# Kernel tuning notes

Measured on AMD Instinct MI355X. Metric: run time of the kernel, lower is better.

Reference implementation:

```python
import jax, jax.numpy as jnp
import numpy as np

B, T = 8, 16384
CLASSES, RC, EC = 256, 32, 256
NLAYERS = 40          # blocks(4) * layers(10)
DIL = 1024            # source uses 2**layers for every layer (faithful to code)
EPS = 1e-5


def _shift_right(x, d):
    # causal shift: y[t] = x[t-d], zero-padded
    return jnp.pad(x, ((0, 0), (0, 0), (d, 0)))[:, :, : x.shape[-1]]


def _conv1x1(x, w, b):
    # w: [out, in], x: [B, in, T]
    return jnp.einsum('oi,bit->bot', w, x) + b[None, :, None]


def _dconv2(x, w, b, d):
    # causal dilated conv, kernel 2: y[t] = w[:,:,0] x[t-d] + w[:,:,1] x[t] + b
    return (jnp.einsum('oi,bit->bot', w[:, :, 1], x)
            + jnp.einsum('oi,bit->bot', w[:, :, 0], _shift_right(x, d))
            + b[None, :, None])


def _bn(x, g, b):
    # training-mode BatchNorm1d: batch stats over (N, L)
    m = jnp.mean(x, axis=(0, 2), keepdims=True)
    v = jnp.var(x, axis=(0, 2), keepdims=True)
    return (x - m) * jax.lax.rsqrt(v + EPS) * g[None, :, None] + b[None, :, None]


def _mish(x):
    return x * jnp.tanh(jax.nn.softplus(x))


def setup_inputs() -> dict:
    key = jax.random.key(0)
    ks = jax.random.split(key, 16)
    n = jax.random.normal
    return {
        'x': n(ks[0], (B, CLASSES, T), jnp.float32),
        'start_w': n(ks[1], (RC, CLASSES), jnp.float32) * 0.05,
        'start_b': n(ks[2], (RC,), jnp.float32) * 0.05,
        'gt_w': n(ks[3], (NLAYERS, RC, RC, 2), jnp.float32) * 0.1,   # tanh branch
        'gt_b': n(ks[4], (NLAYERS, RC), jnp.float32) * 0.05,
        'gs_w': n(ks[5], (NLAYERS, RC, RC, 2), jnp.float32) * 0.1,   # sigmoid branch
        'gs_b': n(ks[6], (NLAYERS, RC), jnp.float32) * 0.05,
        'res_w': n(ks[7], (NLAYERS, RC, RC), jnp.float32) * 0.1,
        'res_b': n(ks[8], (NLAYERS, RC), jnp.float32) * 0.05,
        'bn_g': jnp.ones((NLAYERS, RC), jnp.float32),
        'bn_b': jnp.zeros((NLAYERS, RC), jnp.float32),
        'bn1_g': jnp.ones((RC,), jnp.float32),
        'bn1_b': jnp.zeros((RC,), jnp.float32),
        'e1_w': n(ks[9], (EC, RC), jnp.float32) * 0.1,
        'e1_b': n(ks[10], (EC,), jnp.float32) * 0.05,
        'bn2_g': jnp.ones((EC,), jnp.float32),
        'bn2_b': jnp.zeros((EC,), jnp.float32),
        'e2_w': n(ks[11], (CLASSES, EC), jnp.float32) * 0.05,
        'e2_b': n(ks[12], (CLASSES,), jnp.float32) * 0.05,
    }


def reference(x, start_w, start_b, gt_w, gt_b, gs_w, gs_b, res_w, res_b,
              bn_g, bn_b, bn1_g, bn1_b, e1_w, e1_b, bn2_g, bn2_b, e2_w, e2_b):
    # start_conv: CausalConv(classes, RC, k=1, shift=1) -> 1x1 conv on x shifted right by 1
    h = _conv1x1(_shift_right(x, 1), start_w, start_b)  # [B, RC, T]

    def step(carry, p):
        h, skip = carry
        gtw, gtb, gsw, gsb, rw, rb, bg, bb = p
        g = jnp.tanh(_dconv2(h, gtw, gtb, DIL)) * jax.nn.sigmoid(_dconv2(h, gsw, gsb, DIL))
        skip = skip + g
        h = h + _bn(_conv1x1(g, rw, rb), bg, bb)
        return (h, skip), None

    init = (h, jnp.zeros_like(h))
    (h, skip_sum), _ = jax.lax.scan(
        step, init, (gt_w, gt_b, gs_w, gs_b, res_w, res_b, bn_g, bn_b))

    y = _mish(_bn(skip_sum, bn1_g, bn1_b))
    y = _mish(_bn(_conv1x1(y, e1_w, e1_b), bn2_g, bn2_b))
    return _conv1x1(y, e2_w, e2_b)  # [B, CLASSES, T]
```

## Files before the change

### kernel.cpp

```cpp
#include <hip/hip_runtime.h>


#define EPSV 1e-5f
#define RN   (1.f/131072.f)

#define H_OFF  0
#define SK_OFF (4*1024*1024)
#define ST_OFF (8*1024*1024)
#define ST_SKIP 2560
#define ST_MU   2624
#define ST_Y    2656
#define ST_A2   3680
#define ST_B2   3936
#define ST_TOT  4192

__device__ __forceinline__ float rcp_f(float x) { return __builtin_amdgcn_rcpf(x); }
__device__ __forceinline__ float tanh_f(float x) {
    float e = __expf(2.f * x);
    return 1.f - 2.f * rcp_f(e + 1.f);
}
__device__ __forceinline__ float sigm_f(float x) { return rcp_f(1.f + __expf(-x)); }
__device__ __forceinline__ float mish_f(float x) {
    float e = __expf(x);
    float sp = (x > 15.f) ? x : __logf(1.f + e);
    return x * tanh_f(sp);
}

__global__ void k_zero(float* __restrict__ st) {
    int i = blockIdx.x * 256 + threadIdx.x;
    if (i < ST_TOT) st[i] = 0.f;
}

__global__ __launch_bounds__(256) void k_start(
        const float* __restrict__ x, const float* __restrict__ sw_g,
        const float* __restrict__ sb_g, float* __restrict__ h, float* __restrict__ skip)
{
    __shared__ float sw[256*36];
    __shared__ float sb[32];
    int tid = threadIdx.x, blk = blockIdx.x;
    int b = blk >> 6, r0 = (blk & 63) << 4;
    for (int k = tid; k < 8192; k += 256) {
        int o = k >> 8, c = k & 255;
        sw[c*36 + o] = sw_g[k];
    }
    if (tid < 32) sb[tid] = sb_g[tid];
    __syncthreads();

    int rr = tid & 15, s = tid >> 4;
    int t = r0 + rr + (s << 10);
    bool valid = (t >= 1);
    const float* xr = x + (long)b*256*16384 + (valid ? (t-1) : 0);
    float acc[32];
    #pragma unroll
    for (int o = 0; o < 32; ++o) acc[o] = 0.f;
    for (int c = 0; c < 256; ++c) {
        float xv = xr[(long)c*16384];
        xv = valid ? xv : 0.f;
        const float4* wrow = (const float4*)&sw[c*36];
        #pragma unroll
        for (int o4 = 0; o4 < 8; ++o4) {
            float4 w = wrow[o4];
            acc[o4*4+0] += w.x*xv; acc[o4*4+1] += w.y*xv;
            acc[o4*4+2] += w.z*xv; acc[o4*4+3] += w.w*xv;
        }
    }
    __syncthreads();
    #pragma unroll
    for (int o = 0; o < 32; ++o) sw[(rr*32 + o)*16 + s] = acc[o] + sb[o];
    __syncthreads();
    float4* hd = (float4*)(h + (long)blk*8192);
    float4* sd = (float4*)(skip + (long)blk*8192);
    const float4* ss = (const float4*)sw;
    float4 z4 = make_float4(0.f, 0.f, 0.f, 0.f);
    for (int k = tid; k < 2048; k += 256) { hd[k] = ss[k]; sd[k] = z4; }
}

__global__ __launch_bounds__(256) void k_layer(
        const float* __restrict__ gt_w, const float* __restrict__ gt_b,
        const float* __restrict__ gs_w, const float* __restrict__ gs_b,
        const float* __restrict__ res_w, const float* __restrict__ res_b,
        const float* __restrict__ bn_g, const float* __restrict__ bn_b,
        float* __restrict__ h, float* __restrict__ z, float* __restrict__ skip,
        float* __restrict__ st, int L)
{
    __shared__ float s_w[4096];
    __shared__ float s_r[1024];
    __shared__ float s_hg[4096];
    __shared__ float s_red[4][32][2];

    int tid = threadIdx.x;
    int o = tid & 31, chl = tid >> 5;
    long base = (long)blockIdx.x*4096 + chl*512 + o*16;

    for (int k = tid; k < 1024; k += 256) {
        int oo = k >> 5, ii = k & 31;
        float2 a = ((const float2*)(gt_w + (long)L*2048))[k];
        float2 c = ((const float2*)(gs_w + (long)L*2048))[k];
        float* d = &s_w[(ii*32 + oo)*4];
        d[0] = a.x; d[1] = a.y; d[2] = c.x; d[3] = c.y;
        s_r[ii*32 + oo] = res_w[(long)L*1024 + k];
    }

    float hreg[16];
    float4* hp4 = (float4*)(h + base);
    #pragma unroll
    for (int q = 0; q < 4; ++q) {
        float4 t4 = hp4[q];
        hreg[4*q+0]=t4.x; hreg[4*q+1]=t4.y; hreg[4*q+2]=t4.z; hreg[4*q+3]=t4.w;
    }
    if (L > 0) {
        float ssum = st[(L-1)*64 + o], ssq = st[(L-1)*64 + 32 + o];
        float m = ssum * RN;
        float v = ssq * RN - m*m;
        float a = rsqrtf(v + EPSV) * bn_g[(L-1)*32 + o];
        float bb = bn_b[(L-1)*32 + o] - m*a;
        const float4* zp4 = (const float4*)(z + base);
        #pragma unroll
        for (int q = 0; q < 4; ++q) {
            float4 t4 = zp4[q];
            hreg[4*q+0] += t4.x*a + bb; hreg[4*q+1] += t4.y*a + bb;
            hreg[4*q+2] += t4.z*a + bb; hreg[4*q+3] += t4.w*a + bb;
        }
        #pragma unroll
        for (int q = 0; q < 4; ++q)
            hp4[q] = make_float4(hreg[4*q], hreg[4*q+1], hreg[4*q+2], hreg[4*q+3]);
    }
    float4* hs4 = (float4*)&s_hg[chl*512 + o*16];
    #pragma unroll
    for (int q = 0; q < 4; ++q)
        hs4[q] = make_float4(hreg[4*q], hreg[4*q+1], hreg[4*q+2], hreg[4*q+3]);
    __syncthreads();

    float aT[16], aS[16];
    float gtb = gt_b[L*32 + o], gsb = gs_b[L*32 + o];
    #pragma unroll
    for (int s = 0; s < 16; ++s) { aT[s] = gtb; aS[s] = gsb; }
    #pragma unroll 4
    for (int i = 0; i < 32; ++i) {
        float4 w = *(const float4*)&s_w[(i*32 + o)*4];
        const float4* hr = (const float4*)&s_hg[chl*512 + i*16];
        float hp = 0.f;
        #pragma unroll
        for (int s4 = 0; s4 < 4; ++s4) {
            float4 hv = hr[s4];
            int s = 4*s4;
            aT[s+0] += w.y*hv.x + w.x*hp;   aS[s+0] += w.w*hv.x + w.z*hp;
            aT[s+1] += w.y*hv.y + w.x*hv.x; aS[s+1] += w.w*hv.y + w.z*hv.x;
            aT[s+2] += w.y*hv.z + w.x*hv.y; aS[s+2] += w.w*hv.z + w.z*hv.y;
            aT[s+3] += w.y*hv.w + w.x*hv.z; aS[s+3] += w.w*hv.w + w.z*hv.z;
            hp = hv.w;
        }
    }
    float g[16], sk[16];
    #pragma unroll
    for (int s = 0; s < 16; ++s) g[s] = tanh_f(aT[s]) * sigm_f(aS[s]);

    float4* skp4 = (float4*)(skip + base);
    #pragma unroll
    for (int q = 0; q < 4; ++q) {
        float4 t4 = skp4[q];
        sk[4*q+0] = t4.x + g[4*q+0]; sk[4*q+1] = t4.y + g[4*q+1];
        sk[4*q+2] = t4.z + g[4*q+2]; sk[4*q+3] = t4.w + g[4*q+3];
        skp4[q] = make_float4(sk[4*q], sk[4*q+1], sk[4*q+2], sk[4*q+3]);
    }

    __syncthreads();
    #pragma unroll
    for (int q = 0; q < 4; ++q)
        hs4[q] = make_float4(g[4*q], g[4*q+1], g[4*q+2], g[4*q+3]);
    __syncthreads();

    float az[16];
    float rbv = res_b[L*32 + o];
    #pragma unroll
    for (int s = 0; s < 16; ++s) az[s] = rbv;
    #pragma unroll 4
    for (int i = 0; i < 32; ++i) {
        float w = s_r[i*32 + o];
        const float4* gr = (const float4*)&s_hg[chl*512 + i*16];
        #pragma unroll
        for (int s4 = 0; s4 < 4; ++s4) {
            float4 gv = gr[s4];
            az[4*s4+0] += w*gv.x; az[4*s4+1] += w*gv.y;
            az[4*s4+2] += w*gv.z; az[4*s4+3] += w*gv.w;
        }
    }
    float4* zp4w = (float4*)(z + base);
    #pragma unroll
    for (int q = 0; q < 4; ++q)
        zp4w[q] = make_float4(az[4*q], az[4*q+1], az[4*q+2], az[4*q+3]);

    float ps = 0.f, pq = 0.f;
    #pragma unroll
    for (int s = 0; s < 16; ++s) { ps += az[s]; pq += az[s]*az[s]; }
    ps += __shfl_down(ps, 32); pq += __shfl_down(pq, 32);
    int wv = tid >> 6;
    if ((tid & 63) < 32) { s_red[wv][o][0] = ps; s_red[wv][o][1] = pq; }
    __syncthreads();
    if (tid < 32) {
        float a = s_red[0][tid][0] + s_red[1][tid][0] + s_red[2][tid][0] + s_red[3][tid][0];
        atomicAdd(&st[L*64 + tid], a);
    } else if (tid < 64) {
        int c = tid - 32;
        float a = s_red[0][c][1] + s_red[1][c][1] + s_red[2][c][1] + s_red[3][c][1];
        atomicAdd(&st[L*64 + 32 + c], a);
    }

    if (L == 39) {
        float p2 = 0.f, q2 = 0.f;
        #pragma unroll
        for (int s = 0; s < 16; ++s) { p2 += sk[s]; q2 += sk[s]*sk[s]; }
        p2 += __shfl_down(p2, 32); q2 += __shfl_down(q2, 32);
        __syncthreads();
        if ((tid & 63) < 32) { s_red[wv][o][0] = p2; s_red[wv][o][1] = q2; }
        __syncthreads();
        if (tid < 32) {
            float a = s_red[0][tid][0] + s_red[1][tid][0] + s_red[2][tid][0] + s_red[3][tid][0];
            atomicAdd(&st[ST_SKIP + tid], a);
        } else if (tid < 64) {
            int c = tid - 32;
            float a = s_red[0][c][1] + s_red[1][c][1] + s_red[2][c][1] + s_red[3][c][1];
            atomicAdd(&st[ST_SKIP + 32 + c], a);
        }
    }
}

__global__ __launch_bounds__(256) void k_ep_a(
        const float* __restrict__ skip, const float* __restrict__ bn1_g,
        const float* __restrict__ bn1_b, float* __restrict__ st)
{
    __shared__ float sy[256*33];
    __shared__ float sA[32], sB[32];
    int tid = threadIdx.x;
    long cb = (long)blockIdx.x * 8192;
    if (tid < 32) {
        float ssum = st[ST_SKIP + tid], ssq = st[ST_SKIP + 32 + tid];
        float m = ssum * RN, v = ssq * RN - m*m;
        float a = rsqrtf(v + EPSV) * bn1_g[tid];
        sA[tid] = a; sB[tid] = bn1_b[tid] - m*a;
    }
    __syncthreads();
    for (int k = tid; k < 8192; k += 256) {
        int i = k & 31, p = k >> 5;
        int rr = p & 15, s = p >> 4;
        float v = skip[cb + rr*512 + i*16 + s];
        sy[p*33 + i] = mish_f(v * sA[i] + sB[i]);
    }
    __syncthreads();
    if (tid < 32) {
        float mu = 0.f;
        for (int p = 0; p < 256; ++p) mu += sy[p*33 + tid];
        atomicAdd(&st[ST_MU + tid], mu);
    }
    int jj = tid & 31, i0 = tid >> 5;
    float a0 = 0.f, a1 = 0.f, a2 = 0.f, a3 = 0.f;
    for (int p = 0; p < 256; ++p) {
        float yj = sy[p*33 + jj];
        a0 += yj * sy[p*33 + i0];
        a1 += yj * sy[p*33 + i0 + 8];
        a2 += yj * sy[p*33 + i0 + 16];
        a3 += yj * sy[p*33 + i0 + 24];
    }
    atomicAdd(&st[ST_Y + (i0     )*32 + jj], a0);
    atomicAdd(&st[ST_Y + (i0 +  8)*32 + jj], a1);
    atomicAdd(&st[ST_Y + (i0 + 16)*32 + jj], a2);
    atomicAdd(&st[ST_Y + (i0 + 24)*32 + jj], a3);
}

__global__ void k_ep_b(
        const float* __restrict__ e1_w, const float* __restrict__ e1_b,
        const float* __restrict__ bn2_g, const float* __restrict__ bn2_b,
        float* __restrict__ st)
{
    __shared__ float mu[32];
    int o = threadIdx.x;
    if (o < 32) mu[o] = st[ST_MU + o] * RN;
    __syncthreads();
    float w[32];
    const float4* wr = (const float4*)(e1_w + o*32);
    #pragma unroll
    for (int q = 0; q < 8; ++q) {
        float4 t4 = wr[q];
        w[4*q]=t4.x; w[4*q+1]=t4.y; w[4*q+2]=t4.z; w[4*q+3]=t4.w;
    }
    float m2 = e1_b[o];
    #pragma unroll
    for (int i = 0; i < 32; ++i) m2 += w[i]*mu[i];
    float var = 0.f;
    for (int i = 0; i < 32; ++i) {
        float wi = w[i], mi = mu[i];
        for (int j = 0; j < 32; ++j)
            var += wi * w[j] * (st[ST_Y + i*32 + j]*RN - mi*mu[j]);
    }
    float a2 = rsqrtf(var + EPSV) * bn2_g[o];
    st[ST_A2 + o] = a2;
    st[ST_B2 + o] = bn2_b[o] - m2*a2;
}

__global__ __launch_bounds__(256, 4) void k_ep_c(
        const float* __restrict__ skip,
        const float* __restrict__ bn1_g, const float* __restrict__ bn1_b,
        const float* __restrict__ e1_w, const float* __restrict__ e1_b,
        const float* __restrict__ e2_w, const float* __restrict__ e2_b,
        const float* __restrict__ st, float* __restrict__ out)
{
    __shared__ float y1l[32*32];
    __shared__ float y2l[256*36];
    __shared__ float sA[32], sB[32];
    int tid = threadIdx.x;
    int blk = blockIdx.x;
    int b = blk >> 6, r0 = (blk & 63) << 4;
    long cb = (long)blk * 8192;
    if (tid < 32) {
        float ssum = st[ST_SKIP + tid], ssq = st[ST_SKIP + 32 + tid];
        float m = ssum * RN, v = ssq * RN - m*m;
        float a = rsqrtf(v + EPSV) * bn1_g[tid];
        sA[tid] = a; sB[tid] = bn1_b[tid] - m*a;
    }
    float w1[32];
    {
        const float4* wr = (const float4*)(e1_w + tid*32);
        #pragma unroll
        for (int q = 0; q < 8; ++q) {
            float4 t4 = wr[q];
            w1[4*q]=t4.x; w1[4*q+1]=t4.y; w1[4*q+2]=t4.z; w1[4*q+3]=t4.w;
        }
    }
    float a2 = st[ST_A2 + tid], b2 = st[ST_B2 + tid];
    float eb1 = e1_b[tid];
    float eb2 = e2_b[tid];
    const float4* w2row = (const float4*)(e2_w + (long)tid * 256);
    __syncthreads();

    for (int st8 = 0; st8 < 8; ++st8) {
        for (int k = tid; k < 1024; k += 256) {
            int i = k >> 5, q = k & 31;
            int rr = q & 15, sl = q >> 4;
            float v = skip[cb + rr*512 + i*16 + st8*2 + sl];
            y1l[i*32 + q] = mish_f(v * sA[i] + sB[i]);
        }
        __syncthreads();
        #pragma unroll 2
        for (int q4 = 0; q4 < 8; ++q4) {
            float4 acc = make_float4(eb1, eb1, eb1, eb1);
            #pragma unroll 8
            for (int i = 0; i < 32; ++i) {
                float4 yv = *(const float4*)&y1l[i*32 + q4*4];
                float wi = w1[i];
                acc.x += wi*yv.x; acc.y += wi*yv.y; acc.z += wi*yv.z; acc.w += wi*yv.w;
            }
            float4 y2v;
            y2v.x = mish_f(acc.x*a2 + b2);
            y2v.y = mish_f(acc.y*a2 + b2);
            y2v.z = mish_f(acc.z*a2 + b2);
            y2v.w = mish_f(acc.w*a2 + b2);
            *(float4*)&y2l[tid*36 + q4*4] = y2v;
        }
        __syncthreads();
        float acc[32];
        #pragma unroll
        for (int q = 0; q < 32; ++q) acc[q] = eb2;
        for (int i4 = 0; i4 < 64; ++i4) {
            float4 w4 = w2row[i4];
            float wa[4] = {w4.x, w4.y, w4.z, w4.w};
            #pragma unroll
            for (int ii = 0; ii < 4; ++ii) {
                float wv = wa[ii];
                const float* yr = &y2l[(i4*4 + ii)*36];
                #pragma unroll
                for (int q4 = 0; q4 < 8; ++q4) {
                    float4 yv = *(const float4*)&yr[q4*4];
                    acc[q4*4+0] += wv*yv.x; acc[q4*4+1] += wv*yv.y;
                    acc[q4*4+2] += wv*yv.z; acc[q4*4+3] += wv*yv.w;
                }
            }
        }
        long ob = ((long)b*256 + tid)*16384 + (long)(st8*2)*1024 + r0;
        float4* op = (float4*)&out[ob];
        op[0] = make_float4(acc[0],  acc[1],  acc[2],  acc[3]);
        op[1] = make_float4(acc[4],  acc[5],  acc[6],  acc[7]);
        op[2] = make_float4(acc[8],  acc[9],  acc[10], acc[11]);
        op[3] = make_float4(acc[12], acc[13], acc[14], acc[15]);
        float4* op2 = (float4*)&out[ob + 1024];
        op2[0] = make_float4(acc[16], acc[17], acc[18], acc[19]);
        op2[1] = make_float4(acc[20], acc[21], acc[22], acc[23]);
        op2[2] = make_float4(acc[24], acc[25], acc[26], acc[27]);
        op2[3] = make_float4(acc[28], acc[29], acc[30], acc[31]);
    }
}

extern "C" void kernel_launch(void* const* d_in, const int* in_sizes, int n_in,
                              void* d_out, int out_size, void* d_ws, size_t ws_size,
                              hipStream_t stream) {
    const float* x       = (const float*)d_in[0];
    const float* start_w = (const float*)d_in[1];
    const float* start_b = (const float*)d_in[2];
    const float* gt_w    = (const float*)d_in[3];
    const float* gt_b    = (const float*)d_in[4];
    const float* gs_w    = (const float*)d_in[5];
    const float* gs_b    = (const float*)d_in[6];
    const float* res_w   = (const float*)d_in[7];
    const float* res_b   = (const float*)d_in[8];
    const float* bn_g    = (const float*)d_in[9];
    const float* bn_b    = (const float*)d_in[10];
    const float* bn1_g   = (const float*)d_in[11];
    const float* bn1_b   = (const float*)d_in[12];
    const float* e1_w    = (const float*)d_in[13];
    const float* e1_b    = (const float*)d_in[14];
    const float* bn2_g   = (const float*)d_in[15];
    const float* bn2_b   = (const float*)d_in[16];
    const float* e2_w    = (const float*)d_in[17];
    const float* e2_b    = (const float*)d_in[18];
    float* ws  = (float*)d_ws;
    float* out = (float*)d_out;

    float* h    = ws + H_OFF;
    float* skip = ws + SK_OFF;
    float* st   = ws + ST_OFF;
    size_t need_full = ((size_t)ST_OFF + 8192 + 4*1024*1024) * 4;
    float* z = (ws_size >= need_full) ? (ws + ST_OFF + 8192)
                                      : (float*)d_out;

    k_zero<<<dim3(17), dim3(256), 0, stream>>>(st);
    k_start<<<dim3(512), dim3(256), 0, stream>>>(x, start_w, start_b, h, skip);
    for (int L = 0; L < 40; ++L)
        k_layer<<<dim3(1024), dim3(256), 0, stream>>>(
            gt_w, gt_b, gs_w, gs_b, res_w, res_b, bn_g, bn_b, h, z, skip, st, L);
    k_ep_a<<<dim3(512), dim3(256), 0, stream>>>(skip, bn1_g, bn1_b, st);
    k_ep_b<<<dim3(1), dim3(256), 0, stream>>>(e1_w, e1_b, bn2_g, bn2_b, st);
    k_ep_c<<<dim3(512), dim3(256), 0, stream>>>(skip, bn1_g, bn1_b, e1_w, e1_b,
                                                e2_w, e2_b, st, out);
}
```

Baseline: 2.646 ms.

## Fuse all 40 residual layers into one persistent cooperative kernel with grid sync

Replaces the 40 per-layer launches with one cooperative persistent kernel. Each block keeps its h, skip and residual-conv activations in registers across layers, and exchanges BatchNorm statistics through slotted atomics in a scratch area placed in the output buffer, separated by grid.sync. This removes the per-layer global round trips for h, z and skip and the launch overhead. In exchange it depends on 512 blocks of 512 threads all being co-resident, and it pays for a grid-wide barrier every layer. The epilogue kernel is also split into two half-work blocks and now computes the bn1 scale per element.

```diff
diff --git a/kernel.cpp b/kernel.cpp
--- a/kernel.cpp
+++ b/kernel.cpp
@@ -1,4 +1,7 @@
 #include <hip/hip_runtime.h>
+#include <hip/hip_cooperative_groups.h>
+
+namespace cg = cooperative_groups;
 
 
 #define EPSV 1e-5f
@@ -13,6 +16,7 @@
 #define ST_A2   3680
 #define ST_B2   3936
 #define ST_TOT  4192
+#define LST_N   (40*8*64)
 
 __device__ __forceinline__ float rcp_f(float x) { return __builtin_amdgcn_rcpf(x); }
 __device__ __forceinline__ float tanh_f(float x) {
@@ -26,9 +30,9 @@
     return x * tanh_f(sp);
 }
 
-__global__ void k_zero(float* __restrict__ st) {
+__global__ void k_zero(float* __restrict__ p, int n) {
     int i = blockIdx.x * 256 + threadIdx.x;
-    if (i < ST_TOT) st[i] = 0.f;
+    if (i < n) p[i] = 0.f;
 }
 
 __global__ __launch_bounds__(256) void k_start(
@@ -73,6 +77,178 @@
     const float4* ss = (const float4*)sw;
     float4 z4 = make_float4(0.f, 0.f, 0.f, 0.f);
     for (int k = tid; k < 2048; k += 256) { hd[k] = ss[k]; sd[k] = z4; }
+}
+
+__global__ __launch_bounds__(512, 4) void k_fused(
+        const float* __restrict__ gt_w, const float* __restrict__ gt_b,
+        const float* __restrict__ gs_w, const float* __restrict__ gs_b,
+        const float* __restrict__ res_w, const float* __restrict__ res_b,
+        const float* __restrict__ bn_g, const float* __restrict__ bn_b,
+        const float* __restrict__ h, float* __restrict__ skip,
+        float* __restrict__ st, float* __restrict__ lst)
+{
+    __shared__ float s_w[4096];
+    __shared__ float s_r[1024];
+    __shared__ float s_hg[8192];
+    __shared__ float s_red[8][32][2];
+    __shared__ float s_ab[64];
+
+    int tid = threadIdx.x;
+    int o = tid & 31, chl = tid >> 5;
+    long base = (long)blockIdx.x*8192 + chl*512 + o*16;
+    int slot = blockIdx.x & 7;
+
+    float hreg[16], sk[16], zr[16];
+    {
+        const float4* hp4 = (const float4*)(h + base);
+        #pragma unroll
+        for (int q = 0; q < 4; ++q) {
+            float4 t4 = hp4[q];
+            hreg[4*q+0]=t4.x; hreg[4*q+1]=t4.y; hreg[4*q+2]=t4.z; hreg[4*q+3]=t4.w;
+        }
+    }
+    #pragma unroll
+    for (int s = 0; s < 16; ++s) sk[s] = 0.f;
+
+    cg::grid_group grid = cg::this_grid();
+
+    for (int L = 0; L < 40; ++L) {
+        for (int k = tid; k < 1024; k += 512) {
+            int oo = k >> 5, ii = k & 31;
+            float2 a = ((const float2*)(gt_w + (long)L*2048))[k];
+            float2 c = ((const float2*)(gs_w + (long)L*2048))[k];
+            float* d = &s_w[(ii*32 + oo)*4];
+            d[0] = a.x; d[1] = a.y; d[2] = c.x; d[3] = c.y;
+            s_r[ii*32 + oo] = res_w[(long)L*1024 + k];
+        }
+
+        if (L > 0) {
+            if (tid < 32) {
+                float ssum = 0.f, ssq = 0.f;
+                #pragma unroll
+                for (int r = 0; r < 8; ++r) {
+                    ssum += __hip_atomic_load(&lst[((L-1)*8 + r)*64 + tid],
+                                              __ATOMIC_RELAXED, __HIP_MEMORY_SCOPE_AGENT);
+                    ssq  += __hip_atomic_load(&lst[((L-1)*8 + r)*64 + 32 + tid],
+                                              __ATOMIC_RELAXED, __HIP_MEMORY_SCOPE_AGENT);
+                }
+                float m = ssum * RN;
+                float v = ssq * RN - m*m;
+                float a = rsqrtf(v + EPSV) * bn_g[(L-1)*32 + tid];
+                s_ab[tid] = a;
+                s_ab[32 + tid] = bn_b[(L-1)*32 + tid] - m*a;
+            }
+            __syncthreads();
+            float a = s_ab[o], bb = s_ab[32 + o];
+            #pragma unroll
+            for (int s = 0; s < 16; ++s) hreg[s] += zr[s]*a + bb;
+        }
+
+        float4* hs4 = (float4*)&s_hg[chl*512 + o*16];
+        #pragma unroll
+        for (int q = 0; q < 4; ++q)
+            hs4[q] = make_float4(hreg[4*q], hreg[4*q+1], hreg[4*q+2], hreg[4*q+3]);
+        __syncthreads();
+
+        float aT[16], aS[16];
+        float gtb = gt_b[L*32 + o], gsb = gs_b[L*32 + o];
+        #pragma unroll
+        for (int s = 0; s < 16; ++s) { aT[s] = gtb; aS[s] = gsb; }
+        #pragma unroll 4
+        for (int i = 0; i < 32; ++i) {
+            float4 w = *(const float4*)&s_w[(i*32 + o)*4];
+            const float4* hr = (const float4*)&s_hg[chl*512 + i*16];
+            float hp = 0.f;
+            #pragma unroll
+            for (int s4 = 0; s4 < 4; ++s4) {
+                float4 hv = hr[s4];
+                int s = 4*s4;
+                aT[s+0] += w.y*hv.x + w.x*hp;   aS[s+0] += w.w*hv.x + w.z*hp;
+                aT[s+1] += w.y*hv.y + w.x*hv.x; aS[s+1] += w.w*hv.y + w.z*hv.x;
+                aT[s+2] += w.y*hv.z + w.x*hv.y; aS[s+2] += w.w*hv.z + w.z*hv.y;
+                aT[s+3] += w.y*hv.w + w.x*hv.z; aS[s+3] += w.w*hv.w + w.z*hv.z;
+                hp = hv.w;
+            }
+        }
+        float g[16];
+        #pragma unroll
+        for (int s = 0; s < 16; ++s) {
+            g[s] = tanh_f(aT[s]) * sigm_f(aS[s]);
+            sk[s] += g[s];
+        }
+
+        if (L < 39) {
+            __syncthreads();
+            #pragma unroll
+            for (int q = 0; q < 4; ++q)
+                hs4[q] = make_float4(g[4*q], g[4*q+1], g[4*q+2], g[4*q+3]);
+            __syncthreads();
+
+            float rbv = res_b[L*32 + o];
+            #pragma unroll
+            for (int s = 0; s < 16; ++s) zr[s] = rbv;
+            #pragma unroll 4
+            for (int i = 0; i < 32; ++i) {
+                float w = s_r[i*32 + o];
+                const float4* gr = (const float4*)&s_hg[chl*512 + i*16];
+                #pragma unroll
+                for (int s4 = 0; s4 < 4; ++s4) {
+                    float4 gv = gr[s4];
+                    zr[4*s4+0] += w*gv.x; zr[4*s4+1] += w*gv.y;
+                    zr[4*s4+2] += w*gv.z; zr[4*s4+3] += w*gv.w;
+                }
+            }
+
+            float ps = 0.f, pq = 0.f;
+            #pragma unroll
+            for (int s = 0; s < 16; ++s) { ps += zr[s]; pq += zr[s]*zr[s]; }
+            ps += __shfl_down(ps, 32); pq += __shfl_down(pq, 32);
+            int wv = tid >> 6;
+            if ((tid & 63) < 32) { s_red[wv][o][0] = ps; s_red[wv][o][1] = pq; }
+            __syncthreads();
+            if (tid < 32) {
+                float a = 0.f;
+                #pragma unroll
+                for (int w8 = 0; w8 < 8; ++w8) a += s_red[w8][tid][0];
+                atomicAdd(&lst[(L*8 + slot)*64 + tid], a);
+            } else if (tid < 64) {
+                int c = tid - 32;
+                float a = 0.f;
+                #pragma unroll
+                for (int w8 = 0; w8 < 8; ++w8) a += s_red[w8][c][1];
+                atomicAdd(&lst[(L*8 + slot)*64 + 32 + c], a);
+            }
+            grid.sync();
+        }
+    }
+
+    {
+        float4* skp4 = (float4*)(skip + base);
+        #pragma unroll
+        for (int q = 0; q < 4; ++q)
+            skp4[q] = make_float4(sk[4*q], sk[4*q+1], sk[4*q+2], sk[4*q+3]);
+
+        float p2 = 0.f, q2 = 0.f;
+        #pragma unroll
+        for (int s = 0; s < 16; ++s) { p2 += sk[s]; q2 += sk[s]*sk[s]; }
+        p2 += __shfl_down(p2, 32); q2 += __shfl_down(q2, 32);
+        int wv = tid >> 6;
+        __syncthreads();
+        if ((tid & 63) < 32) { s_red[wv][o][0] = p2; s_red[wv][o][1] = q2; }
+        __syncthreads();
+        if (tid < 32) {
+            float a = 0.f;
+            #pragma unroll
+            for (int w8 = 0; w8 < 8; ++w8) a += s_red[w8][tid][0];
+            atomicAdd(&st[ST_SKIP + tid], a);
+        } else if (tid < 64) {
+            int c = tid - 32;
+            float a = 0.f;
+            #pragma unroll
+            for (int w8 = 0; w8 < 8; ++w8) a += s_red[w8][c][1];
+            atomicAdd(&st[ST_SKIP + 32 + c], a);
+        }
+    }
 }
 
 __global__ __launch_bounds__(256) void k_layer(
@@ -306,17 +482,11 @@
 {
     __shared__ float y1l[32*32];
     __shared__ float y2l[256*36];
-    __shared__ float sA[32], sB[32];
     int tid = threadIdx.x;
-    int blk = blockIdx.x;
+    int blk2 = blockIdx.x;
+    int blk = blk2 >> 1, half = blk2 & 1;
     int b = blk >> 6, r0 = (blk & 63) << 4;
     long cb = (long)blk * 8192;
-    if (tid < 32) {
-        float ssum = st[ST_SKIP + tid], ssq = st[ST_SKIP + 32 + tid];
-        float m = ssum * RN, v = ssq * RN - m*m;
-        float a = rsqrtf(v + EPSV) * bn1_g[tid];
-        sA[tid] = a; sB[tid] = bn1_b[tid] - m*a;
-    }
     float w1[32];
     {
         const float4* wr = (const float4*)(e1_w + tid*32);
@@ -330,14 +500,17 @@
     float eb1 = e1_b[tid];
     float eb2 = e2_b[tid];
     const float4* w2row = (const float4*)(e2_w + (long)tid * 256);
-    __syncthreads();
-
-    for (int st8 = 0; st8 < 8; ++st8) {
+
+    for (int st8 = half*4; st8 < half*4 + 4; ++st8) {
         for (int k = tid; k < 1024; k += 256) {
             int i = k >> 5, q = k & 31;
+            float ssum = st[ST_SKIP + i], ssq = st[ST_SKIP + 32 + i];
+            float m = ssum * RN, vv = ssq * RN - m*m;
+            float a1 = rsqrtf(vv + EPSV) * bn1_g[i];
+            float b1 = bn1_b[i] - m*a1;
             int rr = q & 15, sl = q >> 4;
             float v = skip[cb + rr*512 + i*16 + st8*2 + sl];
-            y1l[i*32 + q] = mish_f(v * sA[i] + sB[i]);
+            y1l[i*32 + q] = mish_f(v * a1 + b1);
         }
         __syncthreads();
         #pragma unroll 2
@@ -417,17 +590,44 @@
     float* h    = ws + H_OFF;
     float* skip = ws + SK_OFF;
     float* st   = ws + ST_OFF;
-    size_t need_full = ((size_t)ST_OFF + 8192 + 4*1024*1024) * 4;
-    float* z = (ws_size >= need_full) ? (ws + ST_OFF + 8192)
-                                      : (float*)d_out;
-
-    k_zero<<<dim3(17), dim3(256), 0, stream>>>(st);
+    float* lst  = out;
+
+    int coop_ok = 0;
+    {
+        int dev = 0, attr = 0, occ = 0;
+        if (hipGetDevice(&dev) == hipSuccess &&
+            hipDeviceGetAttribute(&attr, hipDeviceAttributeCooperativeLaunch, dev)
+                == hipSuccess && attr) {
+            if (hipOccupancyMaxActiveBlocksPerMultiprocessor(&occ, k_fused, 512, 0)
+                    == hipSuccess && occ >= 2)
+                coop_ok = 1;
+        }
+    }
+
+    k_zero<<<dim3(17), dim3(256), 0, stream>>>(st, ST_TOT);
+    k_zero<<<dim3(80), dim3(256), 0, stream>>>(lst, LST_N);
     k_start<<<dim3(512), dim3(256), 0, stream>>>(x, start_w, start_b, h, skip);
-    for (int L = 0; L < 40; ++L)
-        k_layer<<<dim3(1024), dim3(256), 0, stream>>>(
-            gt_w, gt_b, gs_w, gs_b, res_w, res_b, bn_g, bn_b, h, z, skip, st, L);
+
+    if (coop_ok) {
+        void* kargs[12] = {
+            (void*)&gt_w, (void*)&gt_b, (void*)&gs_w, (void*)&gs_b,
+            (void*)&res_w, (void*)&res_b, (void*)&bn_g, (void*)&bn_b,
+            (void*)&h, (void*)&skip, (void*)&st, (void*)&lst };
+        if (hipLaunchCooperativeKernel(k_fused, dim3(512), dim3(512),
+                                       kargs, 0, stream) != hipSuccess)
+            coop_ok = 0;
+    }
+    if (!coop_ok) {
+        size_t need_full = ((size_t)ST_OFF + 8192 + 4*1024*1024) * 4;
+        float* z = (ws_size >= need_full) ? (ws + ST_OFF + 8192)
+                                          : (float*)d_out;
+        for (int L = 0; L < 40; ++L)
+            k_layer<<<dim3(1024), dim3(256), 0, stream>>>(
+                gt_w, gt_b, gs_w, gs_b, res_w, res_b, bn_g, bn_b, h, z, skip, st, L);
+    }
+
     k_ep_a<<<dim3(512), dim3(256), 0, stream>>>(skip, bn1_g, bn1_b, st);
     k_ep_b<<<dim3(1), dim3(256), 0, stream>>>(e1_w, e1_b, bn2_g, bn2_b, st);
-    k_ep_c<<<dim3(512), dim3(256), 0, stream>>>(skip, bn1_g, bn1_b, e1_w, e1_b,
-                                                e2_w, e2_b, st, out);
-}
+    k_ep_c<<<dim3(1024), dim3(256), 0, stream>>>(skip, bn1_g, bn1_b, e1_w, e1_b,
+                                                 e2_w, e2_b, st, out);
+}
```

New measurement: 2.611 ms. Within noise of the previous version (-1.3%).
